# Kernel tuning notes

Hardware: AMD Instinct MI355X
Metric: run time of the kernel (lower is better)

The kernel has to match this reference:

```python
import jax, jax.numpy as jnp
import numpy as np

B, S, D, E, H, K = 2, 2048, 1024, 8, 4096, 2


def setup_inputs() -> dict:
    key = jax.random.key(0)
    ks = jax.random.split(key, 8)
    w = lambda i, shape: jax.random.normal(ks[i], shape, jnp.float32) * 0.02
    return {
        "x": jax.random.normal(ks[0], (B, S, D), jnp.float32),
        "noise": jax.random.normal(ks[1], (B, S, E), jnp.float32),
        "Wg": w(2, (E, D)),
        "noise_weight": jnp.zeros((E,), jnp.float32),
        "W1": w(3, (E, D, H)),
        "b1": jnp.zeros((E, H), jnp.float32),
        "W2": w(4, (E, D, H)),
        "b2": jnp.zeros((E, H), jnp.float32),
        "Wp": w(5, (E, H, D)),
        "bp": jnp.zeros((E, D), jnp.float32),
        "k": K,
    }


def reference(x, noise, Wg, noise_weight, W1, b1, W2, b2, Wp, bp, k):
    Bb, Ss, Dd = x.shape
    Ee = Wg.shape[0]
    # --- noisy top-k gate (noisy_std = 1.0) ---
    logits = jnp.einsum('bsd,ed->bse', x, Wg)
    noisy = logits + noise * noise_weight            # [B,S,E]
    vals, idx = jax.lax.top_k(noisy, k)              # [B,S,k]
    oh = jax.nn.one_hot(idx, Ee, dtype=x.dtype)      # [B,S,k,E]
    sel = oh.sum(axis=-2) > 0                        # [B,S,E] selected mask
    scat = (oh * vals[..., None]).sum(axis=-2)       # scatter topk logits
    sparse = jnp.where(sel, scat, -jnp.inf)
    gate = jax.nn.softmax(sparse, axis=-1)           # zero weight off-topk
    # --- dense-equivalent expert compute (gate==0 off top-k => same math as masked dispatch) ---
    xf = x.reshape(Bb * Ss, Dd)                      # [T,D]
    gf = gate.reshape(Bb * Ss, Ee)                   # [T,E]
    h1 = jnp.einsum('td,edh->eth', xf, W1) + b1[:, None, :]
    h2 = jnp.einsum('td,edh->eth', xf, W2) + b2[:, None, :]
    hh = h1 * jax.nn.silu(h2)                        # SwiGLU
    outs = jnp.einsum('eth,ehd->etd', hh, Wp) + bp[:, None, :]
    final = jnp.einsum('etd,te->td', outs, gf).reshape(Bb, Ss, Dd)
    return final, idx
```

## Files before the change

### kernel.cpp

```cpp
#include <hip/hip_runtime.h>
#include <math.h>

#define Bc 2
#define Sc 2048
#define Dc 1024
#define Ec 8
#define Hc 4096
#define Tc (Bc*Sc)
#define NSLOT (Tc*2)
#define FINAL_N ((size_t)Tc*Dc)
#define BK 32

typedef float f32x4 __attribute__((ext_vector_type(4)));
typedef __bf16 bf16x8 __attribute__((ext_vector_type(8)));

__device__ __forceinline__ unsigned short f2bf(float f) {
    union { float f; unsigned int u; } v; v.f = f;
    return (unsigned short)((v.u + 0x7fffu + ((v.u >> 16) & 1u)) >> 16);
}

__device__ __forceinline__ void gload16(const unsigned short* g, unsigned short* l) {
    __builtin_amdgcn_global_load_lds(
        (const __attribute__((address_space(1))) unsigned int*)g,
        (__attribute__((address_space(3))) unsigned int*)l,
        16, 0, 0);
}

__device__ __forceinline__ void fence_bar() {
    __builtin_amdgcn_sched_barrier(0);
    asm volatile("s_barrier" ::: "memory");
    __builtin_amdgcn_sched_barrier(0);
}

__global__ void k_cvt_x(const float* __restrict__ x, unsigned short* __restrict__ xbf) {
    int gid = blockIdx.x * 256 + threadIdx.x;
    const float4* p = (const float4*)x + (size_t)gid * 2;
    float4 a = p[0], b = p[1];
    ushort4 r0 = { f2bf(a.x), f2bf(a.y), f2bf(a.z), f2bf(a.w) };
    ushort4 r1 = { f2bf(b.x), f2bf(b.y), f2bf(b.z), f2bf(b.w) };
    ushort4* o = (ushort4*)xbf + (size_t)gid * 2;
    o[0] = r0; o[1] = r1;
}

__global__ void k_transpose_cvt2(const float* __restrict__ inA, const float* __restrict__ inB,
                                 unsigned short* __restrict__ outA, unsigned short* __restrict__ outB,
                                 int R, int C, int nz_per_mat) {
    __shared__ float tile[64][65];
    int z = blockIdx.z;
    const float* in; unsigned short* out;
    if (z < nz_per_mat) { in = inA; out = outA; }
    else { in = inB; out = outB; z -= nz_per_mat; }
    size_t base = (size_t)z * (size_t)R * C;
    int cb = blockIdx.x * 64, rb = blockIdx.y * 64;
    int t = threadIdx.x;
    int q = t & 15, g = t >> 4;
    #pragma unroll
    for (int j = 0; j < 4; j++) {
        int row = g + 16*j;
        float4 v = *(const float4*)&in[base + (size_t)(rb+row)*C + cb + q*4];
        tile[row][q*4+0] = v.x; tile[row][q*4+1] = v.y;
        tile[row][q*4+2] = v.z; tile[row][q*4+3] = v.w;
    }
    __syncthreads();
    #pragma unroll
    for (int j = 0; j < 4; j++) {
        int co = g + 16*j;
        ushort4 o;
        o.x = f2bf(tile[q*4+0][co]); o.y = f2bf(tile[q*4+1][co]);
        o.z = f2bf(tile[q*4+2][co]); o.w = f2bf(tile[q*4+3][co]);
        *(ushort4*)&out[base + (size_t)(cb+co)*R + rb + q*4] = o;
    }
}

__global__ void k_gate(const float* __restrict__ x, const float* __restrict__ noise,
                       const float* __restrict__ Wg, const float* __restrict__ nw,
                       float* __restrict__ out_idx, int* __restrict__ counts,
                       int* __restrict__ tok_top, float* __restrict__ tok_w) {
    int t = blockIdx.x;
    int lane = threadIdx.x;
    const float* xr = x + (size_t)t * Dc;
    double acc[Ec];
    #pragma unroll
    for (int e = 0; e < Ec; e++) acc[e] = 0.0;
    for (int i = 0; i < Dc/64; i++) {
        int d = lane + i*64;
        double xv = (double)xr[d];
        #pragma unroll
        for (int e = 0; e < Ec; e++) acc[e] += xv * (double)Wg[e*Dc + d];
    }
    #pragma unroll
    for (int e = 0; e < Ec; e++)
        for (int off = 32; off > 0; off >>= 1)
            acc[e] += __shfl_down(acc[e], off);
    if (lane == 0) {
        double noisy[Ec];
        #pragma unroll
        for (int e = 0; e < Ec; e++)
            noisy[e] = acc[e] + (double)noise[t*Ec + e] * (double)nw[e];
        int i0 = 0;
        for (int e = 1; e < Ec; e++) if (noisy[e] > noisy[i0]) i0 = e;
        int i1 = -1;
        for (int e = 0; e < Ec; e++) {
            if (e == i0) continue;
            if (i1 < 0 || noisy[e] > noisy[i1]) i1 = e;
        }
        double ee = exp(noisy[i1] - noisy[i0]);
        float w0 = (float)(1.0 / (1.0 + ee));
        float w1 = (float)(ee / (1.0 + ee));
        out_idx[t*2 + 0] = (float)i0;
        out_idx[t*2 + 1] = (float)i1;
        tok_top[t*2] = i0; tok_top[t*2+1] = i1;
        tok_w[t*2] = w0;   tok_w[t*2+1] = w1;
        atomicAdd(&counts[i0], 1);
        atomicAdd(&counts[i1], 1);
    }
}

__global__ void k_scan(const int* __restrict__ counts, int* __restrict__ offsets) {
    if (threadIdx.x == 0) {
        int s = 0;
        for (int e = 0; e < Ec; e++) { offsets[e] = s; s += counts[e]; }
        offsets[Ec] = s;
    }
}

__global__ void k_fill(const int* __restrict__ tok_top, const int* __restrict__ offsets,
                       int* __restrict__ fill, int* __restrict__ slot_token,
                       int* __restrict__ slot_of) {
    int t = blockIdx.x * 256 + threadIdx.x;
    if (t >= Tc) return;
    #pragma unroll
    for (int j = 0; j < 2; j++) {
        int e = tok_top[t*2 + j];
        int pos = atomicAdd(&fill[e], 1);
        int slot = offsets[e] + pos;
        slot_token[slot] = t;
        slot_of[t*2 + j] = slot;
    }
}

#define BM1 256
#define BN1 128
#define A1SZ (BM1*BK)
#define W1SZ (BN1*BK)

__global__ __launch_bounds__(512, 2) void k_gemm1(
    const unsigned short* __restrict__ xbf,
    const unsigned short* __restrict__ w1t, const unsigned short* __restrict__ w2t,
    const float* __restrict__ b1, const float* __restrict__ b2,
    const int* __restrict__ counts, const int* __restrict__ offsets,
    const int* __restrict__ slot_token,
    unsigned short* __restrict__ hh) {
    int e = blockIdx.z;
    int n_e = counts[e];
    int m0 = blockIdx.y * BM1;
    if (m0 >= n_e) return;
    int base = offsets[e];
    int n0 = blockIdx.x * BN1;

    __shared__ __align__(16) unsigned short sA[3*A1SZ];
    __shared__ __align__(16) unsigned short sW1[3*W1SZ];
    __shared__ __align__(16) unsigned short sW2[3*W1SZ];
    __shared__ int tlist[BM1];

    int tid = threadIdx.x;
    if (tid < BM1) {
        int r = m0 + tid; if (r > n_e - 1) r = n_e - 1;
        tlist[tid] = slot_token[base + r];
    }
    __syncthreads();

    int wid = tid >> 6, lane = tid & 63;
    int wr = wid >> 1, wc = wid & 1;

    int rl = lane >> 2, sc_ = lane & 3;
    int rA0 = wid*32 + rl, rA1 = rA0 + 16;
    int rB  = wid*16 + rl;
    int cA0 = sc_ ^ ((rA0 >> 1) & 3);
    int cA1 = sc_ ^ ((rA1 >> 1) & 3);
    int cB  = sc_ ^ ((rB  >> 1) & 3);
    int tA0 = tlist[rA0], tA1 = tlist[rA1];
    const unsigned short* pa0 = xbf + (size_t)tA0*Dc + cA0*8;
    const unsigned short* pa1 = xbf + (size_t)tA1*Dc + cA1*8;
    const size_t wb = ((size_t)e * Hc + n0) * Dc;
    const unsigned short* pw1 = w1t + wb + (size_t)rB*Dc + cB*8;
    const unsigned short* pw2 = w2t + wb + (size_t)rB*Dc + cB*8;
    int aofs = wid*1024, bofs = wid*512;

    f32x4 acc1[4][4], acc2[4][4];
    #pragma unroll
    for (int m = 0; m < 4; m++)
        #pragma unroll
        for (int n = 0; n < 4; n++)
            #pragma unroll
            for (int j = 0; j < 4; j++) { acc1[m][n][j] = 0.0f; acc2[m][n][j] = 0.0f; }

    int arow = lane & 15, cr = lane >> 4;

    auto STAGE_A = [&](int buf, int kk) {
        unsigned short* d = sA + buf*A1SZ + aofs;
        gload16(pa0 + kk, d);
        gload16(pa1 + kk, d + 512);
    };
    auto STAGE_W = [&](int buf, int kk) {
        gload16(pw1 + kk, sW1 + buf*W1SZ + bofs);
        gload16(pw2 + kk, sW2 + buf*W1SZ + bofs);
    };

    STAGE_A(0, 0);  STAGE_W(0, 0);
    STAGE_A(1, BK); STAGE_W(1, BK);

    const int NT = Dc / BK;
    int ib = 0;
    for (int t = 0; t < NT; ++t) {
        int is = ib + 2; if (is >= 3) is -= 3;
        if (t + 2 < NT) {
            STAGE_A(is, (t+2)*BK);
            asm volatile("s_waitcnt vmcnt(6)" ::: "memory");
        } else if (t + 1 < NT) {
            asm volatile("s_waitcnt vmcnt(4)" ::: "memory");
        } else {
            asm volatile("s_waitcnt vmcnt(0)" ::: "memory");
        }
        fence_bar();
        const unsigned short* lA = sA  + ib*A1SZ;
        const unsigned short* l1 = sW1 + ib*W1SZ;
        const unsigned short* l2 = sW2 + ib*W1SZ;
        bf16x8 af[4], w1f[4], w2f[4];
        #pragma unroll
        for (int m = 0; m < 4; m++) {
            int rr = wr*64 + m*16 + arow;
            int cc = cr ^ ((rr >> 1) & 3);
            af[m] = *(const bf16x8*)&lA[rr*BK + cc*8];
        }
        #pragma unroll
        for (int n = 0; n < 4; n++) {
            int rr = wc*64 + n*16 + arow;
            int cc = cr ^ ((rr >> 1) & 3);
            w1f[n] = *(const bf16x8*)&l1[rr*BK + cc*8];
        }
        if (t + 2 < NT) STAGE_W(is, (t+2)*BK);
        asm volatile("s_waitcnt lgkmcnt(0)" ::: "memory");
        fence_bar();
        __builtin_amdgcn_s_setprio(1);
        #pragma unroll
        for (int m = 0; m < 4; m++)
            #pragma unroll
            for (int n = 0; n < 4; n++)
                acc1[m][n] = __builtin_amdgcn_mfma_f32_16x16x32_bf16(af[m], w1f[n], acc1[m][n], 0, 0, 0);
        #pragma unroll
        for (int n = 0; n < 4; n++) {
            int rr = wc*64 + n*16 + arow;
            int cc = cr ^ ((rr >> 1) & 3);
            w2f[n] = *(const bf16x8*)&l2[rr*BK + cc*8];
        }
        #pragma unroll
        for (int m = 0; m < 4; m++)
            #pragma unroll
            for (int n = 0; n < 4; n++)
                acc2[m][n] = __builtin_amdgcn_mfma_f32_16x16x32_bf16(af[m], w2f[n], acc2[m][n], 0, 0, 0);
        __builtin_amdgcn_s_setprio(0);
        ib = ib + 1; if (ib == 3) ib = 0;
    }

    int lrow = (lane >> 4) * 4, lcol = lane & 15;
    #pragma unroll
    for (int n = 0; n < 4; n++) {
        int hcol = n0 + wc*64 + n*16 + lcol;
        float bias1 = b1[e*Hc + hcol], bias2 = b2[e*Hc + hcol];
        #pragma unroll
        for (int m = 0; m < 4; m++) {
            int rb = m0 + wr*64 + m*16 + lrow;
            #pragma unroll
            for (int j = 0; j < 4; j++) {
                int r = rb + j;
                if (r < n_e) {
                    float h1v = acc1[m][n][j] + bias1;
                    float h2v = acc2[m][n][j] + bias2;
                    float hhv = h1v * (h2v / (1.0f + expf(-h2v)));
                    hh[(size_t)(base + r)*Hc + hcol] = f2bf(hhv);
                }
            }
        }
    }
}

#define BM2 256
#define BN2 128
#define A2SZ (BM2*BK)
#define B2SZ (BN2*BK)

__global__ __launch_bounds__(512, 2) void k_gemm2(
    const unsigned short* __restrict__ hh,
    const unsigned short* __restrict__ wpt,
    const float* __restrict__ bp,
    const int* __restrict__ counts, const int* __restrict__ offsets,
    float* __restrict__ outb) {
    int e = blockIdx.z;
    int n_e = counts[e];
    int m0 = blockIdx.y * BM2;
    if (m0 >= n_e) return;
    int base = offsets[e];
    int n0 = blockIdx.x * BN2;

    __shared__ __align__(16) unsigned short sA[3*2*A2SZ];
    __shared__ __align__(16) unsigned short sB[3*2*B2SZ];

    int tid = threadIdx.x;
    int wid = tid >> 6, lane = tid & 63;
    int wr = wid >> 1, wc = wid & 1;

    int rl = lane >> 2, sc_ = lane & 3;
    int rA0 = wid*32 + rl, rA1 = rA0 + 16;
    int rB  = wid*16 + rl;
    int cA0 = sc_ ^ ((rA0 >> 1) & 3);
    int cA1 = sc_ ^ ((rA1 >> 1) & 3);
    int cB  = sc_ ^ ((rB  >> 1) & 3);
    int gr0 = m0 + rA0; if (gr0 > n_e - 1) gr0 = n_e - 1;
    int gr1 = m0 + rA1; if (gr1 > n_e - 1) gr1 = n_e - 1;
    const unsigned short* pa0 = hh + (size_t)(base + gr0)*Hc + cA0*8;
    const unsigned short* pa1 = hh + (size_t)(base + gr1)*Hc + cA1*8;
    const unsigned short* pb  = wpt + ((size_t)e*Dc + n0 + rB)*Hc + cB*8;
    int aofs = wid*1024, bofs = wid*512;

    f32x4 acc[4][4];
    #pragma unroll
    for (int m = 0; m < 4; m++)
        #pragma unroll
        for (int n = 0; n < 4; n++)
            #pragma unroll
            for (int j = 0; j < 4; j++) acc[m][n][j] = 0.0f;

    int arow = lane & 15, cr = lane >> 4;

    auto STAGE_A = [&](int buf, int kk) {
        unsigned short* d = sA + buf*(2*A2SZ) + aofs;
        gload16(pa0 + kk, d);            gload16(pa1 + kk, d + 512);
        gload16(pa0 + kk + BK, d + A2SZ); gload16(pa1 + kk + BK, d + A2SZ + 512);
    };
    auto STAGE_B = [&](int buf, int kk) {
        unsigned short* d = sB + buf*(2*B2SZ) + bofs;
        gload16(pb + kk, d);
        gload16(pb + kk + BK, d + B2SZ);
    };

    STAGE_A(0, 0);  STAGE_B(0, 0);
    STAGE_A(1, 64); STAGE_B(1, 64);

    const int NT = Hc / 64;
    int ib = 0;
    for (int t = 0; t < NT; ++t) {
        int is = ib + 2; if (is >= 3) is -= 3;
        if (t + 2 < NT) {
            STAGE_A(is, (t+2)*64);
            asm volatile("s_waitcnt vmcnt(10)" ::: "memory");
        } else if (t + 1 < NT) {
            asm volatile("s_waitcnt vmcnt(6)" ::: "memory");
        } else {
            asm volatile("s_waitcnt vmcnt(0)" ::: "memory");
        }
        fence_bar();
        const unsigned short* lA0 = sA + ib*(2*A2SZ);
        const unsigned short* lA1 = lA0 + A2SZ;
        const unsigned short* lB0 = sB + ib*(2*B2SZ);
        const unsigned short* lB1 = lB0 + B2SZ;
        bf16x8 af[2][4], wf[2][4];
        #pragma unroll
        for (int m = 0; m < 4; m++) {
            int rr = wr*64 + m*16 + arow;
            int cc = cr ^ ((rr >> 1) & 3);
            af[0][m] = *(const bf16x8*)&lA0[rr*BK + cc*8];
            af[1][m] = *(const bf16x8*)&lA1[rr*BK + cc*8];
        }
        #pragma unroll
        for (int n = 0; n < 4; n++) {
            int rr = wc*64 + n*16 + arow;
            int cc = cr ^ ((rr >> 1) & 3);
            wf[0][n] = *(const bf16x8*)&lB0[rr*BK + cc*8];
        }
        if (t + 2 < NT) STAGE_B(is, (t+2)*64);
        asm volatile("s_waitcnt lgkmcnt(0)" ::: "memory");
        fence_bar();
        __builtin_amdgcn_s_setprio(1);
        #pragma unroll
        for (int m = 0; m < 4; m++)
            #pragma unroll
            for (int n = 0; n < 4; n++)
                acc[m][n] = __builtin_amdgcn_mfma_f32_16x16x32_bf16(af[0][m], wf[0][n], acc[m][n], 0, 0, 0);
        #pragma unroll
        for (int n = 0; n < 4; n++) {
            int rr = wc*64 + n*16 + arow;
            int cc = cr ^ ((rr >> 1) & 3);
            wf[1][n] = *(const bf16x8*)&lB1[rr*BK + cc*8];
        }
        #pragma unroll
        for (int m = 0; m < 4; m++)
            #pragma unroll
            for (int n = 0; n < 4; n++)
                acc[m][n] = __builtin_amdgcn_mfma_f32_16x16x32_bf16(af[1][m], wf[1][n], acc[m][n], 0, 0, 0);
        __builtin_amdgcn_s_setprio(0);
        ib = ib + 1; if (ib == 3) ib = 0;
    }

    int lrow = (lane >> 4) * 4, lcol = lane & 15;
    #pragma unroll
    for (int n = 0; n < 4; n++) {
        int dcol = n0 + wc*64 + n*16 + lcol;
        float bias = bp[e*Dc + dcol];
        #pragma unroll
        for (int m = 0; m < 4; m++) {
            int rb = m0 + wr*64 + m*16 + lrow;
            #pragma unroll
            for (int j = 0; j < 4; j++) {
                int r = rb + j;
                if (r < n_e)
                    outb[(size_t)(base + r)*Dc + dcol] = acc[m][n][j] + bias;
            }
        }
    }
}

__global__ void k_combine(const float* __restrict__ outb, const int* __restrict__ slot_of,
                          const float* __restrict__ tok_w, float* __restrict__ final_out) {
    int gid = blockIdx.x * 256 + threadIdx.x;
    int t = gid >> 8;
    int c = (gid & 255) * 4;
    int s0 = slot_of[t*2], s1 = slot_of[t*2 + 1];
    float w0 = tok_w[t*2], w1 = tok_w[t*2 + 1];
    float4 o0 = *(const float4*)&outb[(size_t)s0*Dc + c];
    float4 o1 = *(const float4*)&outb[(size_t)s1*Dc + c];
    float4 r;
    r.x = w0*o0.x + w1*o1.x;
    r.y = w0*o0.y + w1*o1.y;
    r.z = w0*o0.z + w1*o1.z;
    r.w = w0*o0.w + w1*o1.w;
    *(float4*)&final_out[(size_t)t*Dc + c] = r;
}

extern "C" void kernel_launch(void* const* d_in, const int* in_sizes, int n_in,
                              void* d_out, int out_size, void* d_ws, size_t ws_size,
                              hipStream_t stream) {
    (void)in_sizes; (void)n_in; (void)out_size; (void)ws_size;
    const float* x     = (const float*)d_in[0];
    const float* noise = (const float*)d_in[1];
    const float* Wg    = (const float*)d_in[2];
    const float* nw    = (const float*)d_in[3];
    const float* W1    = (const float*)d_in[4];
    const float* b1    = (const float*)d_in[5];
    const float* W2    = (const float*)d_in[6];
    const float* b2    = (const float*)d_in[7];
    const float* Wp    = (const float*)d_in[8];
    const float* bp    = (const float*)d_in[9];

    char* ws = (char*)d_ws;
    size_t off = 0;
    unsigned short* XBF = (unsigned short*)(ws + off); off += (size_t)Tc*Dc*2;
    unsigned short* W1T = (unsigned short*)(ws + off); off += (size_t)Ec*Dc*Hc*2;
    unsigned short* W2T = (unsigned short*)(ws + off); off += (size_t)Ec*Dc*Hc*2;
    unsigned short* WPT = (unsigned short*)(ws + off); off += (size_t)Ec*Hc*Dc*2;
    unsigned short* HH  = (unsigned short*)(ws + off); off += (size_t)NSLOT*Hc*2;
    float*          OUTB= (float*)(ws + off);          off += (size_t)NSLOT*Dc*4;
    int*   counts    = (int*)(ws + off);
    int*   fill      = (int*)(ws + off + 32);
    int*   offsets   = (int*)(ws + off + 64);
    int*   tok_top   = (int*)(ws + off + 128);
    float* tok_w     = (float*)(ws + off + 128 + (size_t)Tc*2*4);
    int*   slot_token= (int*)(ws + off + 128 + (size_t)Tc*2*8);
    int*   slot_of   = (int*)(ws + off + 128 + (size_t)Tc*2*8 + (size_t)NSLOT*4);

    float* final_out = (float*)d_out;
    float* idx_out   = (float*)d_out + FINAL_N;

    hipMemsetAsync(counts, 0, 64, stream);

    k_cvt_x<<<(Tc*Dc/8)/256, 256, 0, stream>>>(x, XBF);
    k_transpose_cvt2<<<dim3(Hc/64, Dc/64, 2*Ec), 256, 0, stream>>>(W1, W2, W1T, W2T, Dc, Hc, Ec);
    k_transpose_cvt2<<<dim3(Dc/64, Hc/64, Ec), 256, 0, stream>>>(Wp, Wp, WPT, WPT, Hc, Dc, Ec);

    k_gate<<<Tc, 64, 0, stream>>>(x, noise, Wg, nw, idx_out, counts, tok_top, tok_w);
    k_scan<<<1, 64, 0, stream>>>(counts, offsets);
    k_fill<<<Tc/256, 256, 0, stream>>>(tok_top, offsets, fill, slot_token, slot_of);

    k_gemm1<<<dim3(Hc/BN1, Tc/BM1, Ec), 512, 0, stream>>>(XBF, W1T, W2T, b1, b2,
                                                          counts, offsets, slot_token, HH);
    k_gemm2<<<dim3(Dc/BN2, Tc/BM2, Ec), 512, 0, stream>>>(HH, WPT, bp, counts, offsets, OUTB);
    k_combine<<<(Tc*Dc/4)/256, 256, 0, stream>>>(OUTB, slot_of, tok_w, final_out);
}
```

Baseline: 682.7 us.

## Register double-buffer LDS fragments and software-pipeline both MoE GEMM mainloops

Both expert GEMM kernels now preload the next K-slice's LDS fragments into a second register set while the MFMAs for the current slice run. This removes the second barrier and the LDS-read stall that came before each MFMA batch. The loop is unrolled by two with ping-pong fragment registers, and swizzled LDS offsets are precomputed once. GEMM2 also moves from BK=64 stages to BK=32, which halves its shared memory, though it adds loop iterations and register pressure from the doubled fragments.

```diff
diff --git a/kernel.cpp b/kernel.cpp
--- a/kernel.cpp
+++ b/kernel.cpp
@@ -196,71 +196,69 @@
             for (int j = 0; j < 4; j++) { acc1[m][n][j] = 0.0f; acc2[m][n][j] = 0.0f; }
 
     int arow = lane & 15, cr = lane >> 4;
-
-    auto STAGE_A = [&](int buf, int kk) {
-        unsigned short* d = sA + buf*A1SZ + aofs;
-        gload16(pa0 + kk, d);
-        gload16(pa1 + kk, d + 512);
-    };
-    auto STAGE_W = [&](int buf, int kk) {
+    int ccf = cr ^ ((arow >> 1) & 3);
+    int offA[4], offW[4];
+    #pragma unroll
+    for (int m = 0; m < 4; m++) offA[m] = (wr*64 + m*16 + arow)*BK + ccf*8;
+    #pragma unroll
+    for (int n = 0; n < 4; n++) offW[n] = (wc*64 + n*16 + arow)*BK + ccf*8;
+
+    auto STAGE = [&](int buf, int kk) {
+        unsigned short* dA = sA + buf*A1SZ + aofs;
+        gload16(pa0 + kk, dA);
+        gload16(pa1 + kk, dA + 512);
         gload16(pw1 + kk, sW1 + buf*W1SZ + bofs);
         gload16(pw2 + kk, sW2 + buf*W1SZ + bofs);
     };
 
-    STAGE_A(0, 0);  STAGE_W(0, 0);
-    STAGE_A(1, BK); STAGE_W(1, BK);
+#define LDF1(buf, a, w1f, w2f) { \
+    const unsigned short* lA_ = sA  + (buf)*A1SZ; \
+    const unsigned short* l1_ = sW1 + (buf)*W1SZ; \
+    const unsigned short* l2_ = sW2 + (buf)*W1SZ; \
+    _Pragma("unroll") for (int m_ = 0; m_ < 4; m_++) a[m_] = *(const bf16x8*)&lA_[offA[m_]]; \
+    _Pragma("unroll") for (int n_ = 0; n_ < 4; n_++) { \
+        w1f[n_] = *(const bf16x8*)&l1_[offW[n_]]; \
+        w2f[n_] = *(const bf16x8*)&l2_[offW[n_]]; } }
+
+#define MM1(a, w1f, w2f) { \
+    _Pragma("unroll") for (int m_ = 0; m_ < 4; m_++) \
+        _Pragma("unroll") for (int n_ = 0; n_ < 4; n_++) { \
+            acc1[m_][n_] = __builtin_amdgcn_mfma_f32_16x16x32_bf16(a[m_], w1f[n_], acc1[m_][n_], 0, 0, 0); \
+            acc2[m_][n_] = __builtin_amdgcn_mfma_f32_16x16x32_bf16(a[m_], w2f[n_], acc2[m_][n_], 0, 0, 0); } }
+
+    bf16x8 a0[4], x10[4], x20[4], a1[4], x11[4], x21[4];
+
+    STAGE(0, 0); STAGE(1, BK);
+    asm volatile("s_waitcnt vmcnt(4)" ::: "memory");
+    fence_bar();
+    LDF1(0, a0, x10, x20);
+    asm volatile("s_waitcnt lgkmcnt(0)" ::: "memory");
+    __builtin_amdgcn_sched_barrier(0);
 
     const int NT = Dc / BK;
     int ib = 0;
-    for (int t = 0; t < NT; ++t) {
-        int is = ib + 2; if (is >= 3) is -= 3;
-        if (t + 2 < NT) {
-            STAGE_A(is, (t+2)*BK);
-            asm volatile("s_waitcnt vmcnt(6)" ::: "memory");
-        } else if (t + 1 < NT) {
-            asm volatile("s_waitcnt vmcnt(4)" ::: "memory");
-        } else {
-            asm volatile("s_waitcnt vmcnt(0)" ::: "memory");
-        }
-        fence_bar();
-        const unsigned short* lA = sA  + ib*A1SZ;
-        const unsigned short* l1 = sW1 + ib*W1SZ;
-        const unsigned short* l2 = sW2 + ib*W1SZ;
-        bf16x8 af[4], w1f[4], w2f[4];
-        #pragma unroll
-        for (int m = 0; m < 4; m++) {
-            int rr = wr*64 + m*16 + arow;
-            int cc = cr ^ ((rr >> 1) & 3);
-            af[m] = *(const bf16x8*)&lA[rr*BK + cc*8];
-        }
-        #pragma unroll
-        for (int n = 0; n < 4; n++) {
-            int rr = wc*64 + n*16 + arow;
-            int cc = cr ^ ((rr >> 1) & 3);
-            w1f[n] = *(const bf16x8*)&l1[rr*BK + cc*8];
-        }
-        if (t + 2 < NT) STAGE_W(is, (t+2)*BK);
-        asm volatile("s_waitcnt lgkmcnt(0)" ::: "memory");
-        fence_bar();
-        __builtin_amdgcn_s_setprio(1);
-        #pragma unroll
-        for (int m = 0; m < 4; m++)
-            #pragma unroll
-            for (int n = 0; n < 4; n++)
-                acc1[m][n] = __builtin_amdgcn_mfma_f32_16x16x32_bf16(af[m], w1f[n], acc1[m][n], 0, 0, 0);
-        #pragma unroll
-        for (int n = 0; n < 4; n++) {
-            int rr = wc*64 + n*16 + arow;
-            int cc = cr ^ ((rr >> 1) & 3);
-            w2f[n] = *(const bf16x8*)&l2[rr*BK + cc*8];
-        }
-        #pragma unroll
-        for (int m = 0; m < 4; m++)
-            #pragma unroll
-            for (int n = 0; n < 4; n++)
-                acc2[m][n] = __builtin_amdgcn_mfma_f32_16x16x32_bf16(af[m], w2f[n], acc2[m][n], 0, 0, 0);
-        __builtin_amdgcn_s_setprio(0);
-        ib = ib + 1; if (ib == 3) ib = 0;
+
+#define G1ITER(T, CA, CW1, CW2, NA, NW1, NW2) { \
+    int i1_ = ib + 1; if (i1_ == 3) i1_ = 0; \
+    int i2_ = i1_ + 1; if (i2_ == 3) i2_ = 0; \
+    if ((T) + 2 < NT) { \
+        STAGE(i2_, ((T)+2)*BK); \
+        asm volatile("s_waitcnt vmcnt(4)" ::: "memory");    \
+    } else if ((T) + 1 < NT) { \
+        asm volatile("s_waitcnt vmcnt(0)" ::: "memory"); \
+    } \
+    fence_bar();                                 \
+    __builtin_amdgcn_s_setprio(1); \
+    if ((T) + 1 < NT) LDF1(i1_, NA, NW1, NW2);   \
+    MM1(CA, CW1, CW2); \
+    __builtin_amdgcn_s_setprio(0); \
+    asm volatile("s_waitcnt lgkmcnt(0)" ::: "memory"); \
+    __builtin_amdgcn_sched_barrier(0); \
+    ib = i1_; }
+
+    for (int t = 0; t < NT; t += 2) {
+        G1ITER(t,   a0, x10, x20, a1, x11, x21);
+        G1ITER(t+1, a1, x11, x21, a0, x10, x20);
     }
 
     int lrow = (lane >> 4) * 4, lcol = lane & 15;
@@ -270,10 +268,10 @@
         float bias1 = b1[e*Hc + hcol], bias2 = b2[e*Hc + hcol];
         #pragma unroll
         for (int m = 0; m < 4; m++) {
-            int rb = m0 + wr*64 + m*16 + lrow;
+            int rb2 = m0 + wr*64 + m*16 + lrow;
             #pragma unroll
             for (int j = 0; j < 4; j++) {
-                int r = rb + j;
+                int r = rb2 + j;
                 if (r < n_e) {
                     float h1v = acc1[m][n][j] + bias1;
                     float h2v = acc2[m][n][j] + bias2;
@@ -283,6 +281,9 @@
             }
         }
     }
+#undef G1ITER
+#undef MM1
+#undef LDF1
 }
 
 #define BM2 256
@@ -303,8 +304,8 @@
     int base = offsets[e];
     int n0 = blockIdx.x * BN2;
 
-    __shared__ __align__(16) unsigned short sA[3*2*A2SZ];
-    __shared__ __align__(16) unsigned short sB[3*2*B2SZ];
+    __shared__ __align__(16) unsigned short sA[3*A2SZ];
+    __shared__ __align__(16) unsigned short sB[3*B2SZ];
 
     int tid = threadIdx.x;
     int wid = tid >> 6, lane = tid & 63;
@@ -332,74 +333,64 @@
             for (int j = 0; j < 4; j++) acc[m][n][j] = 0.0f;
 
     int arow = lane & 15, cr = lane >> 4;
-
-    auto STAGE_A = [&](int buf, int kk) {
-        unsigned short* d = sA + buf*(2*A2SZ) + aofs;
-        gload16(pa0 + kk, d);            gload16(pa1 + kk, d + 512);
-        gload16(pa0 + kk + BK, d + A2SZ); gload16(pa1 + kk + BK, d + A2SZ + 512);
+    int ccf = cr ^ ((arow >> 1) & 3);
+    int offA[4], offW[4];
+    #pragma unroll
+    for (int m = 0; m < 4; m++) offA[m] = (wr*64 + m*16 + arow)*BK + ccf*8;
+    #pragma unroll
+    for (int n = 0; n < 4; n++) offW[n] = (wc*64 + n*16 + arow)*BK + ccf*8;
+
+    auto STAGE = [&](int buf, int kk) {
+        unsigned short* dA = sA + buf*A2SZ + aofs;
+        gload16(pa0 + kk, dA);
+        gload16(pa1 + kk, dA + 512);
+        gload16(pb  + kk, sB + buf*B2SZ + bofs);
     };
-    auto STAGE_B = [&](int buf, int kk) {
-        unsigned short* d = sB + buf*(2*B2SZ) + bofs;
-        gload16(pb + kk, d);
-        gload16(pb + kk + BK, d + B2SZ);
-    };
-
-    STAGE_A(0, 0);  STAGE_B(0, 0);
-    STAGE_A(1, 64); STAGE_B(1, 64);
-
-    const int NT = Hc / 64;
+
+#define LDF2(buf, a, b) { \
+    const unsigned short* lA_ = sA + (buf)*A2SZ; \
+    const unsigned short* lB_ = sB + (buf)*B2SZ; \
+    _Pragma("unroll") for (int m_ = 0; m_ < 4; m_++) a[m_] = *(const bf16x8*)&lA_[offA[m_]]; \
+    _Pragma("unroll") for (int n_ = 0; n_ < 4; n_++) b[n_] = *(const bf16x8*)&lB_[offW[n_]]; }
+
+#define MM2(a, b) { \
+    _Pragma("unroll") for (int m_ = 0; m_ < 4; m_++) \
+        _Pragma("unroll") for (int n_ = 0; n_ < 4; n_++) \
+            acc[m_][n_] = __builtin_amdgcn_mfma_f32_16x16x32_bf16(a[m_], b[n_], acc[m_][n_], 0, 0, 0); }
+
+    bf16x8 a0[4], b0[4], a1[4], b1f[4];
+
+    STAGE(0, 0); STAGE(1, BK);
+    asm volatile("s_waitcnt vmcnt(3)" ::: "memory");
+    fence_bar();
+    LDF2(0, a0, b0);
+    asm volatile("s_waitcnt lgkmcnt(0)" ::: "memory");
+    __builtin_amdgcn_sched_barrier(0);
+
+    const int NT = Hc / BK;
     int ib = 0;
-    for (int t = 0; t < NT; ++t) {
-        int is = ib + 2; if (is >= 3) is -= 3;
-        if (t + 2 < NT) {
-            STAGE_A(is, (t+2)*64);
-            asm volatile("s_waitcnt vmcnt(10)" ::: "memory");
-        } else if (t + 1 < NT) {
-            asm volatile("s_waitcnt vmcnt(6)" ::: "memory");
-        } else {
-            asm volatile("s_waitcnt vmcnt(0)" ::: "memory");
-        }
-        fence_bar();
-        const unsigned short* lA0 = sA + ib*(2*A2SZ);
-        const unsigned short* lA1 = lA0 + A2SZ;
-        const unsigned short* lB0 = sB + ib*(2*B2SZ);
-        const unsigned short* lB1 = lB0 + B2SZ;
-        bf16x8 af[2][4], wf[2][4];
-        #pragma unroll
-        for (int m = 0; m < 4; m++) {
-            int rr = wr*64 + m*16 + arow;
-            int cc = cr ^ ((rr >> 1) & 3);
-            af[0][m] = *(const bf16x8*)&lA0[rr*BK + cc*8];
-            af[1][m] = *(const bf16x8*)&lA1[rr*BK + cc*8];
-        }
-        #pragma unroll
-        for (int n = 0; n < 4; n++) {
-            int rr = wc*64 + n*16 + arow;
-            int cc = cr ^ ((rr >> 1) & 3);
-            wf[0][n] = *(const bf16x8*)&lB0[rr*BK + cc*8];
-        }
-        if (t + 2 < NT) STAGE_B(is, (t+2)*64);
-        asm volatile("s_waitcnt lgkmcnt(0)" ::: "memory");
-        fence_bar();
-        __builtin_amdgcn_s_setprio(1);
-        #pragma unroll
-        for (int m = 0; m < 4; m++)
-            #pragma unroll
-            for (int n = 0; n < 4; n++)
-                acc[m][n] = __builtin_amdgcn_mfma_f32_16x16x32_bf16(af[0][m], wf[0][n], acc[m][n], 0, 0, 0);
-        #pragma unroll
-        for (int n = 0; n < 4; n++) {
-            int rr = wc*64 + n*16 + arow;
-            int cc = cr ^ ((rr >> 1) & 3);
-            wf[1][n] = *(const bf16x8*)&lB1[rr*BK + cc*8];
-        }
-        #pragma unroll
-        for (int m = 0; m < 4; m++)
-            #pragma unroll
-            for (int n = 0; n < 4; n++)
-                acc[m][n] = __builtin_amdgcn_mfma_f32_16x16x32_bf16(af[1][m], wf[1][n], acc[m][n], 0, 0, 0);
-        __builtin_amdgcn_s_setprio(0);
-        ib = ib + 1; if (ib == 3) ib = 0;
+
+#define G2ITER(T, CA, CB, NA, NB) { \
+    int i1_ = ib + 1; if (i1_ == 3) i1_ = 0; \
+    int i2_ = i1_ + 1; if (i2_ == 3) i2_ = 0; \
+    if ((T) + 2 < NT) { \
+        STAGE(i2_, ((T)+2)*BK); \
+        asm volatile("s_waitcnt vmcnt(3)" ::: "memory"); \
+    } else if ((T) + 1 < NT) { \
+        asm volatile("s_waitcnt vmcnt(0)" ::: "memory"); \
+    } \
+    fence_bar(); \
+    __builtin_amdgcn_s_setprio(1); \
+    if ((T) + 1 < NT) LDF2(i1_, NA, NB); \
+    MM2(CA, CB); \
+    __builtin_amdgcn_s_setprio(0); \
+    asm volatile("s_waitcnt lgkmcnt(0)" ::: "memory"); \
+    __builtin_amdgcn_sched_barrier(0); \
+    ib = i1_; }
+
+    for (int t = 0; t < NT; t += 2) {
+        G2ITER(t,   a0, b0, a1, b1f);
+        G2ITER(t+1, a1, b1f, a0, b0);
     }
 
     int lrow = (lane >> 4) * 4, lcol = lane & 15;
@@ -409,15 +400,18 @@
         float bias = bp[e*Dc + dcol];
         #pragma unroll
         for (int m = 0; m < 4; m++) {
-            int rb = m0 + wr*64 + m*16 + lrow;
+            int rb2 = m0 + wr*64 + m*16 + lrow;
             #pragma unroll
             for (int j = 0; j < 4; j++) {
-                int r = rb + j;
+                int r = rb2 + j;
                 if (r < n_e)
                     outb[(size_t)(base + r)*Dc + dcol] = acc[m][n][j] + bias;
             }
         }
     }
+#undef G2ITER
+#undef MM2
+#undef LDF2
 }
 
 __global__ void k_combine(const float* __restrict__ outb, const int* __restrict__ slot_of,
```

Result: slower. 703.1 us (+3.0%).
